# Optimization experiments

Measured on AMD Instinct MI355X. Metric: run time of the kernel, lower is better.

The kernel has to match this reference:

```python
import jax, jax.numpy as jnp
import numpy as np

EPS = 1e-6

def _ln2d(x, w, b):
    # LayerNorm2d: normalize over channel dim per pixel
    mu = x.mean(axis=1, keepdims=True)
    var = ((x - mu) ** 2).mean(axis=1, keepdims=True)
    return (x - mu) / jnp.sqrt(var + EPS) * w[None, :, None, None] + b[None, :, None, None]

def _conv1x1(x, w, b):
    return jnp.einsum('oc,bchw->bohw', w, x) + b[None, :, None, None]

def setup_inputs() -> dict:
    key = jax.random.key(0)
    ks = jax.random.split(key, 20)
    B, c, H, W = 4, 32, 256, 256
    dw = 2 * c
    k, wH, wW = 3, 32, 32
    s = 0.05
    d = {}
    d['inp'] = jax.random.normal(ks[0], (B, c, H, W), jnp.float32)
    d['conv2_weight'] = jax.random.normal(ks[1], (B, dw, k, k, wH, wW), jnp.float32) * 0.1
    d['conv1_w'] = jax.random.normal(ks[2], (dw, c), jnp.float32) * s
    d['conv1_b'] = jnp.zeros((dw,), jnp.float32)
    d['conv3_w'] = jax.random.normal(ks[3], (c, c), jnp.float32) * s
    d['conv3_b'] = jnp.zeros((c,), jnp.float32)
    d['sca_w'] = jax.random.normal(ks[4], (c, c), jnp.float32) * s
    d['sca_b'] = jnp.zeros((c,), jnp.float32)
    d['conv4_w'] = jax.random.normal(ks[5], (dw, c), jnp.float32) * s
    d['conv4_b'] = jnp.zeros((dw,), jnp.float32)
    d['conv5_w'] = jax.random.normal(ks[6], (c, c), jnp.float32) * s
    d['conv5_b'] = jnp.zeros((c,), jnp.float32)
    d['norm1_w'] = jnp.ones((c,), jnp.float32)
    d['norm1_b'] = jnp.zeros((c,), jnp.float32)
    d['norm2_w'] = jnp.ones((c,), jnp.float32)
    d['norm2_b'] = jnp.zeros((c,), jnp.float32)
    # original inits these to zero; use small random so the block is non-trivial
    d['beta'] = jax.random.normal(ks[7], (1, c, 1, 1), jnp.float32) * 0.1
    d['gamma'] = jax.random.normal(ks[8], (1, c, 1, 1), jnp.float32) * 0.1
    return d

def reference(inp, conv2_weight, conv1_w, conv1_b, conv3_w, conv3_b, sca_w, sca_b,
              conv4_w, conv4_b, conv5_w, conv5_b, norm1_w, norm1_b, norm2_w, norm2_b,
              beta, gamma):
    B, c, H, W = inp.shape
    x = _ln2d(inp, norm1_w, norm1_b)
    x = _conv1x1(x, conv1_w, conv1_b)                 # [B, 2c, H, W]
    Bw, C, kH, kW, wH, wW = conv2_weight.shape
    # bilinear upsample (half-pixel centers, == torch align_corners=False)
    w2 = conv2_weight.reshape(B * C, kH * kW, wH, wW)
    w2 = jax.image.resize(w2, (B * C, kH * kW, H, W), method='linear')
    w2 = w2.reshape(B, C, kH * kW, H, W)
    # ddf with all-ones channel filter + 'mul' == per-pixel spatial 3x3 conv per channel
    pad = kH // 2
    xp = jnp.pad(x, ((0, 0), (0, 0), (pad, pad), (pad, pad)))
    patches = jnp.stack([xp[:, :, i:i + H, j:j + W]
                         for i in range(kH) for j in range(kW)], axis=2)  # [B,2c,9,H,W]
    x = (patches * w2).sum(axis=2)                    # [B, 2c, H, W]
    x1, x2 = jnp.split(x, 2, axis=1)                  # SimpleGate
    x = x1 * x2                                       # [B, c, H, W]
    s = _conv1x1(x.mean(axis=(2, 3), keepdims=True), sca_w, sca_b)
    x = x * s
    x = _conv1x1(x, conv3_w, conv3_b)
    y = inp + x * beta
    x = _conv1x1(_ln2d(y, norm2_w, norm2_b), conv4_w, conv4_b)
    x1, x2 = jnp.split(x, 2, axis=1)
    x = _conv1x1(x1 * x2, conv5_w, conv5_b)
    return y + x * gamma
```

## Files before the change

### kernel.cpp

```cpp
#include <hip/hip_runtime.h>
#include <hip/hip_bf16.h>

typedef __hip_bfloat16 bf16;
typedef __attribute__((ext_vector_type(8))) unsigned short u16x8;
typedef __attribute__((ext_vector_type(8))) short s16x8;
typedef __attribute__((ext_vector_type(4))) float f32x4;
typedef __attribute__((ext_vector_type(4))) unsigned short us16x4;

#define B_   4
#define C_   32
#define DW_  64
#define H_   256
#define W_   256
#define P_   65536
#define SRC_ 32
#define TRS_ 272
#define TPL_ 70176

#define OW1    0
#define OB1    2048
#define OW3    2112
#define OB3    3136
#define OWS    3168
#define OBS    4192
#define OW4    4224
#define OB4    6272
#define OW5    6336
#define OB5    7360
#define ON1W   7392
#define ON1B   7424
#define ON2W   7456
#define ON2B   7488
#define OBETA  7520
#define OGAMMA 7552
#define OSUMS  7584
#define OSVEC  7712
#define OFLAG  7900
#define CWF_BOFF 32768ull
#define T1_BOFF  (CWF_BOFF + 9437184ull)
#define G_BOFF   (T1_BOFF + 35930112ull)

__device__ __forceinline__ bf16  f2b(float v){ return __float2bfloat16(v); }
__device__ __forceinline__ float bfu(unsigned short u){ return __uint_as_float(((unsigned int)u) << 16); }
__device__ __forceinline__ unsigned short fbits(float v){
    bf16 b = __float2bfloat16(v);
    return *reinterpret_cast<unsigned short*>(&b);
}

template<typename T> __device__ __forceinline__ float ldf(const T* p);
template<> __device__ __forceinline__ float ldf<float>(const float* p){ return *p; }
template<> __device__ __forceinline__ float ldf<bf16>(const bf16* p){ return __bfloat162float(*p); }

template<typename T> __device__ __forceinline__ void stf(T* p, float v);
template<> __device__ __forceinline__ void stf<float>(float* p, float v){ *p = v; }
template<> __device__ __forceinline__ void stf<bf16>(bf16* p, float v){ *p = __float2bfloat16(v); }

template<typename T> struct dtag;
template<> struct dtag<float>{ static constexpr int v = 0; };
template<> struct dtag<bf16>{ static constexpr int v = 1; };

__device__ __forceinline__ f32x4 MF(s16x8 a, s16x8 b, f32x4 c){
    return __builtin_amdgcn_mfma_f32_16x16x32_bf16(a, b, c, 0, 0, 0);
}
__device__ __forceinline__ s16x8 wfrag8(const float* p){
    float4 a = *(const float4*)p;
    float4 c = *(const float4*)(p + 4);
    s16x8 r;
    r[0] = (short)fbits(a.x); r[1] = (short)fbits(a.y);
    r[2] = (short)fbits(a.z); r[3] = (short)fbits(a.w);
    r[4] = (short)fbits(c.x); r[5] = (short)fbits(c.y);
    r[6] = (short)fbits(c.z); r[7] = (short)fbits(c.w);
    return r;
}

__global__ void k_detect(const unsigned short* __restrict__ raw, int* __restrict__ flag)
{
    int t = threadIdx.x;
    int bad = 0;
    for (int k = 0; k < 8; ++k) {
        unsigned short u = raw[2 * (t + 64 * k)];
        float v = __uint_as_float(((unsigned int)u) << 16);
        if (!(fabsf(v) < 1e6f)) bad = 1;
    }
    int anybad = __any(bad);
    if (t == 0) *flag = anybad ? 0 : 1;
}

template<typename T>
__global__ void k_prep(const T* __restrict__ w1, const T* __restrict__ b1,
                       const T* __restrict__ w3, const T* __restrict__ b3,
                       const T* __restrict__ wsc, const T* __restrict__ bsc_,
                       const T* __restrict__ w4, const T* __restrict__ b4,
                       const T* __restrict__ w5, const T* __restrict__ b5,
                       const T* __restrict__ n1w, const T* __restrict__ n1b,
                       const T* __restrict__ n2w, const T* __restrict__ n2b,
                       const T* __restrict__ bet, const T* __restrict__ gam,
                       float* __restrict__ wsf, const int* __restrict__ flag)
{
    if (*flag != dtag<T>::v) return;
    int t = threadIdx.x;
    for (int i = t; i < 2048; i += 256) wsf[OW1 + i] = ldf<T>(w1 + i);
    for (int i = t; i < 64;   i += 256) wsf[OB1 + i] = ldf<T>(b1 + i);
    for (int i = t; i < 1024; i += 256) wsf[OW3 + i] = ldf<T>(w3 + i);
    for (int i = t; i < 32;   i += 256) wsf[OB3 + i] = ldf<T>(b3 + i);
    for (int i = t; i < 1024; i += 256) wsf[OWS + i] = ldf<T>(wsc + i);
    for (int i = t; i < 32;   i += 256) wsf[OBS + i] = ldf<T>(bsc_ + i);
    for (int i = t; i < 2048; i += 256) wsf[OW4 + i] = ldf<T>(w4 + i);
    for (int i = t; i < 64;   i += 256) wsf[OB4 + i] = ldf<T>(b4 + i);
    for (int i = t; i < 1024; i += 256) wsf[OW5 + i] = ldf<T>(w5 + i);
    for (int i = t; i < 32;   i += 256) wsf[OB5 + i] = ldf<T>(b5 + i);
    for (int i = t; i < 32;   i += 256) wsf[ON1W + i] = ldf<T>(n1w + i);
    for (int i = t; i < 32;   i += 256) wsf[ON1B + i] = ldf<T>(n1b + i);
    for (int i = t; i < 32;   i += 256) wsf[ON2W + i] = ldf<T>(n2w + i);
    for (int i = t; i < 32;   i += 256) wsf[ON2B + i] = ldf<T>(n2b + i);
    for (int i = t; i < 32;   i += 256) wsf[OBETA + i] = ldf<T>(bet + i);
    for (int i = t; i < 32;   i += 256) wsf[OGAMMA + i] = ldf<T>(gam + i);
    for (int i = t; i < 128;  i += 256) wsf[OSUMS + i] = 0.f;
}

__global__ void k_cwf(const void* __restrict__ cw, float4* __restrict__ cwf4,
                      const int* __restrict__ flag)
{
    int i4 = blockIdx.x * 256 + threadIdx.x;
    if (*flag == 0) {
        cwf4[i4] = ((const float4*)cw)[i4];
    } else {
        const ushort4* p = (const ushort4*)cw;
        ushort4 v = p[i4];
        cwf4[i4] = make_float4(bfu(v.x), bfu(v.y), bfu(v.z), bfu(v.w));
    }
}

__global__ void k_zpad(unsigned short* __restrict__ t1u)
{
    unsigned short* pl = t1u + (size_t)blockIdx.x * TPL_;
    int t = threadIdx.x;
    for (int i = t; i < 258; i += 256) {
        pl[i] = 0;
        pl[257 * TRS_ + i] = 0;
    }
    pl[(t + 1) * TRS_] = 0;
    pl[(t + 1) * TRS_ + 257] = 0;
}

template<typename T>
__device__ __forceinline__ void ln1_body(const T* __restrict__ inp,
        const float* __restrict__ wsf, bf16* __restrict__ t1p, short* __restrict__ xsh)
{
    const int t = threadIdx.x;
    const int b = blockIdx.x >> 8;
    const int p0 = (blockIdx.x & 255) << 8;

    {
        const T* ip = inp + (size_t)(b * C_) * P_ + p0 + t;
        float v[C_];
        float m = 0.f;
        #pragma unroll
        for (int ch = 0; ch < C_; ++ch) { v[ch] = ldf<T>(ip + (size_t)ch * P_); m += v[ch]; }
        m *= (1.f / C_);
        float var = 0.f;
        #pragma unroll
        for (int ch = 0; ch < C_; ++ch) { float d = v[ch] - m; var += d * d; }
        var *= (1.f / C_);
        float inv = rsqrtf(var + 1e-6f);
        u16x8* xr = (u16x8*)(xsh + t * 32);
        #pragma unroll
        for (int qq = 0; qq < 4; ++qq) {
            u16x8 vv;
            #pragma unroll
            for (int j = 0; j < 8; ++j) {
                int ch = qq * 8 + j;
                vv[j] = fbits((v[ch] - m) * inv * wsf[ON1W + ch] + wsf[ON1B + ch]);
            }
            xr[qq] = vv;
        }
    }
    __syncthreads();

    const int lane = t & 63, wv = t >> 6;
    const int l15 = lane & 15, l4 = lane >> 4;
    const int wp0 = wv * 64;

    s16x8 w1f[4];
    f32x4 b1v[4];
    #pragma unroll
    for (int m = 0; m < 4; ++m) {
        w1f[m] = wfrag8(wsf + OW1 + (m * 16 + l15) * 32 + l4 * 8);
        b1v[m] = *(const f32x4*)(wsf + OB1 + m * 16 + l4 * 4);
    }

    const int h = p0 >> 8;
    bf16* op = t1p + (size_t)(b * DW_) * TPL_ + (size_t)(h + 1) * TRS_ + 1;
    #pragma unroll
    for (int tn = 0; tn < 4; ++tn) {
        int px = wp0 + tn * 16 + l15;
        s16x8 xb = *(const s16x8*)(xsh + px * 32 + l4 * 8);
        #pragma unroll
        for (int m = 0; m < 4; ++m) {
            f32x4 acc = MF(w1f[m], xb, b1v[m]);
            #pragma unroll
            for (int i = 0; i < 4; ++i) {
                int och = m * 16 + l4 * 4 + i;
                op[(size_t)och * TPL_ + px] = f2b(acc[i]);
            }
        }
    }
}

__global__ __launch_bounds__(256, 4) void k_ln1_conv1(const void* __restrict__ inp,
        const float* __restrict__ wsf, bf16* __restrict__ t1p,
        const int* __restrict__ flag)
{
    __shared__ short xsh[256 * 32];
    if (*flag == 0) ln1_body<float>((const float*)inp, wsf, t1p, xsh);
    else            ln1_body<bf16>((const bf16*)inp, wsf, t1p, xsh);
}

#define G_ 4
__global__ __launch_bounds__(256, 4) void k_ddf(const unsigned short* __restrict__ t1u,
        const float* __restrict__ cwf, bf16* __restrict__ g, float* __restrict__ sums)
{
    __shared__ float CWs[4320];

    int bid = blockIdx.x;
    int tile = bid & 31;
    int cg  = (bid >> 5) & 7;
    int b   = bid >> 8;
    int th = tile >> 2, tw = tile & 3;
    int cellh0 = th * 4;
    int cellw0 = tw * 8;
    int cp0 = cg * G_;

    {
        const float* cb = cwf + (size_t)b * (DW_ * 9 * 1024);
        for (int it = 0; it < 17; ++it) {
            int idx = it * 256 + threadIdx.x;
            if (idx < 4320) {
                int cc  = idx % 10;
                int t2  = idx / 10;
                int rr  = t2 % 6;
                int t3  = t2 / 6;
                int tap = t3 % 9;
                int chl = t3 / 9;
                int ch = (chl < G_) ? (cp0 + chl) : (C_ + cp0 + chl - G_);
                int cr = cellh0 - 1 + rr; cr = cr < 0 ? 0 : (cr > 31 ? 31 : cr);
                int cw = cellw0 - 1 + cc; cw = cw < 0 ? 0 : (cw > 31 ? 31 : cw);
                CWs[idx] = cb[ch * 9216 + tap * 1024 + cr * SRC_ + cw];
            }
        }
    }
    __syncthreads();

    int lane = threadIdx.x & 63, wid = threadIdx.x >> 6;
    int k = lane >> 3, r = lane & 7;
    int cellh = cellh0 + wid;
    int h = cellh * 8 + r;
    int w = (cellw0 + k) * 8;

    int rsel = r >> 2;
    float fh = rsel ? ((float)r * 0.125f - 0.4375f) : ((float)r * 0.125f + 0.5625f);
    float gh = 1.f - fh;
    int rr0k = (wid + rsel) * 10 + k;

    const unsigned short* tb = t1u + (size_t)(b * DW_) * TPL_ + (size_t)h * TRS_ + w;
    bf16* gp = g + (size_t)(b * C_) * P_ + h * 256 + w;

    for (int l = 0; l < G_; ++l) {
        int cp = cp0 + l;
        const unsigned short* pl1 = tb + (size_t)cp * TPL_;
        const unsigned short* pl2 = pl1 + (size_t)C_ * TPL_;
        const float* q1 = CWs + l * 540;
        const float* q2 = CWs + (G_ + l) * 540;

        float acc1[8], acc2[8];
        #pragma unroll
        for (int pass = 0; pass < 2; ++pass) {
            const unsigned short* pl = pass ? pl2 : pl1;
            const float* q = pass ? q2 : q1;
            float* acc = pass ? acc2 : acc1;

            u16x8 v8[3];
            unsigned int ve[3];
            #pragma unroll
            for (int i = 0; i < 3; ++i) {
                const unsigned short* rp = pl + i * TRS_;
                v8[i] = *(const u16x8*)rp;
                ve[i] = *(const unsigned int*)(rp + 8);
            }
            float S00[8], S01[8], S10[8], S11[8];
            #pragma unroll
            for (int c = 0; c < 8; ++c) { S00[c]=0.f; S01[c]=0.f; S10[c]=0.f; S11[c]=0.f; }
            #pragma unroll
            for (int i = 0; i < 3; ++i) {
                float p[10];
                #pragma unroll
                for (int j = 0; j < 8; ++j) p[j] = bfu((unsigned short)v8[i][j]);
                p[8] = bfu((unsigned short)(ve[i] & 0xFFFFu));
                p[9] = bfu((unsigned short)(ve[i] >> 16));
                #pragma unroll
                for (int j = 0; j < 3; ++j) {
                    const float* qb = q + (i * 3 + j) * 60 + rr0k;
                    float w00 = qb[0],  w01 = qb[1],  w02 = qb[2];
                    float w10 = qb[10], w11 = qb[11], w12 = qb[12];
                    #pragma unroll
                    for (int c = 0; c < 8; ++c) {
                        float pv = p[c + j];
                        S00[c] += pv * ((c < 4) ? w00 : w01);
                        S01[c] += pv * ((c < 4) ? w01 : w02);
                        S10[c] += pv * ((c < 4) ? w10 : w11);
                        S11[c] += pv * ((c < 4) ? w11 : w12);
                    }
                }
            }
            const float fwt[8] = {0.5625f, 0.6875f, 0.8125f, 0.9375f,
                                  0.0625f, 0.1875f, 0.3125f, 0.4375f};
            #pragma unroll
            for (int c = 0; c < 8; ++c) {
                float fw = fwt[c], gw = 1.f - fw;
                acc[c] = gh * (gw * S00[c] + fw * S01[c]) + fh * (gw * S10[c] + fw * S11[c]);
            }
        }

        u16x8 ov;
        float s = 0.f;
        #pragma unroll
        for (int c = 0; c < 8; ++c) {
            float gv = acc1[c] * acc2[c];
            s += gv;
            bf16 bv = f2b(gv);
            ov[c] = *reinterpret_cast<unsigned short*>(&bv);
        }
        *(u16x8*)(gp + (size_t)cp * P_) = ov;

        #pragma unroll
        for (int off = 32; off >= 1; off >>= 1) s += __shfl_xor(s, off, 64);
        if (lane == 0) atomicAdd(&sums[b * C_ + cp], s);
    }
}

__global__ void k_sca(float* __restrict__ wsf)
{
    int t = threadIdx.x;
    int b = t >> 5, o = t & 31;
    float acc = wsf[OBS + o];
    #pragma unroll
    for (int ch = 0; ch < C_; ++ch)
        acc += wsf[OWS + o * C_ + ch] * (wsf[OSUMS + b * C_ + ch] * (1.f / (float)P_));
    wsf[OSVEC + b * C_ + o] = acc;
}

#define XSTR_ 32
#define ISTR_ 33

template<typename T>
__device__ __forceinline__ void tail_body(const T* __restrict__ inp,
        const bf16* __restrict__ g, const float* __restrict__ wsf,
        T* __restrict__ out, short* __restrict__ xsh, float* __restrict__ ipsh)
{
    const int t = threadIdx.x;
    const int b = blockIdx.x >> 8;
    const int p0 = (blockIdx.x & 255) << 8;

    {
        float sv[32];
        #pragma unroll
        for (int q = 0; q < 8; ++q) {
            float4 v = *(const float4*)(wsf + OSVEC + b * 32 + q * 4);
            sv[4*q+0] = v.x; sv[4*q+1] = v.y; sv[4*q+2] = v.z; sv[4*q+3] = v.w;
        }
        const unsigned short* gp = (const unsigned short*)g + (size_t)(b * C_) * P_ + p0 + t;
        unsigned short row[32];
        #pragma unroll
        for (int ch = 0; ch < C_; ++ch)
            row[ch] = fbits(bfu(gp[(size_t)ch * P_]) * sv[ch]);
        u16x8* xr = (u16x8*)(xsh + t * XSTR_);
        #pragma unroll
        for (int qq = 0; qq < 4; ++qq) {
            u16x8 vv;
            #pragma unroll
            for (int j = 0; j < 8; ++j) vv[j] = row[qq * 8 + j];
            xr[qq] = vv;
        }
        const T* ip = inp + (size_t)(b * C_) * P_ + p0 + t;
        float* ir = ipsh + t * ISTR_;
        #pragma unroll
        for (int ch = 0; ch < C_; ++ch)
            ir[ch] = ldf<T>(ip + (size_t)ch * P_);
    }
    __syncthreads();

    const int lane = t & 63, wv = t >> 6;
    const int l15 = lane & 15, l4 = lane >> 4;
    const int wp0 = wv * 64;

    s16x8 w3f[2], w4f[4];
    #pragma unroll
    for (int m = 0; m < 2; ++m) w3f[m] = wfrag8(wsf + OW3 + (m * 16 + l15) * 32 + l4 * 8);
    #pragma unroll
    for (int m = 0; m < 4; ++m) w4f[m] = wfrag8(wsf + OW4 + (m * 16 + l15) * 32 + l4 * 8);

    f32x4 y[2][4];
    {
        f32x4 b3v[2], btv[2];
        #pragma unroll
        for (int m = 0; m < 2; ++m) {
            b3v[m] = *(const f32x4*)(wsf + OB3   + m * 16 + l4 * 4);
            btv[m] = *(const f32x4*)(wsf + OBETA + m * 16 + l4 * 4);
        }
        #pragma unroll
        for (int tn = 0; tn < 4; ++tn) {
            int px = wp0 + tn * 16 + l15;
            s16x8 xb = *(const s16x8*)(xsh + px * XSTR_ + l4 * 8);
            const float* irr = ipsh + px * ISTR_ + l4 * 4;
            #pragma unroll
            for (int m = 0; m < 2; ++m) {
                f32x4 acc = MF(w3f[m], xb, b3v[m]);
                f32x4 yy;
                #pragma unroll
                for (int i = 0; i < 4; ++i)
                    yy[i] = irr[m * 16 + i] + acc[i] * btv[m][i];
                y[m][tn] = yy;
            }
        }
    }

    {
        f32x4 nwv[2], nbv[2];
        #pragma unroll
        for (int m = 0; m < 2; ++m) {
            nwv[m] = *(const f32x4*)(wsf + ON2W + m * 16 + l4 * 4);
            nbv[m] = *(const f32x4*)(wsf + ON2B + m * 16 + l4 * 4);
        }
        #pragma unroll
        for (int tn = 0; tn < 4; ++tn) {
            float s = 0.f;
            #pragma unroll
            for (int m = 0; m < 2; ++m)
                #pragma unroll
                for (int i = 0; i < 4; ++i) s += y[m][tn][i];
            s += __shfl_xor(s, 16);
            s += __shfl_xor(s, 32);
            float mean = s * (1.f / 32.f);
            float q = 0.f;
            #pragma unroll
            for (int m = 0; m < 2; ++m)
                #pragma unroll
                for (int i = 0; i < 4; ++i) { float d = y[m][tn][i] - mean; q += d * d; }
            q += __shfl_xor(q, 16);
            q += __shfl_xor(q, 32);
            float inv = rsqrtf(q * (1.f / 32.f) + 1e-6f);
            int px = wp0 + tn * 16 + l15;
            #pragma unroll
            for (int m = 0; m < 2; ++m) {
                us16x4 pk;
                #pragma unroll
                for (int i = 0; i < 4; ++i)
                    pk[i] = fbits((y[m][tn][i] - mean) * inv * nwv[m][i] + nbv[m][i]);
                *(us16x4*)(xsh + px * XSTR_ + m * 16 + l4 * 4) = pk;
            }
        }
    }

    {
        f32x4 b4v[4];
        #pragma unroll
        for (int m = 0; m < 4; ++m)
            b4v[m] = *(const f32x4*)(wsf + OB4 + m * 16 + l4 * 4);
        s16x8 yb[4];
        #pragma unroll
        for (int tn = 0; tn < 4; ++tn)
            yb[tn] = *(const s16x8*)(xsh + (wp0 + tn * 16 + l15) * XSTR_ + l4 * 8);
        #pragma unroll
        for (int tn = 0; tn < 4; ++tn) {
            f32x4 a4[4];
            #pragma unroll
            for (int m = 0; m < 4; ++m) a4[m] = MF(w4f[m], yb[tn], b4v[m]);
            int px = wp0 + tn * 16 + l15;
            #pragma unroll
            for (int m = 0; m < 2; ++m) {
                us16x4 pk;
                #pragma unroll
                for (int i = 0; i < 4; ++i) pk[i] = fbits(a4[m][i] * a4[m + 2][i]);
                *(us16x4*)(xsh + px * XSTR_ + m * 16 + l4 * 4) = pk;
            }
        }
    }

    {
        s16x8 w5f[2];
        #pragma unroll
        for (int m = 0; m < 2; ++m) w5f[m] = wfrag8(wsf + OW5 + (m * 16 + l15) * 32 + l4 * 8);
        f32x4 b5v[2], gmv[2];
        #pragma unroll
        for (int m = 0; m < 2; ++m) {
            b5v[m] = *(const f32x4*)(wsf + OB5    + m * 16 + l4 * 4);
            gmv[m] = *(const f32x4*)(wsf + OGAMMA + m * 16 + l4 * 4);
        }
        s16x8 ub[4];
        #pragma unroll
        for (int tn = 0; tn < 4; ++tn)
            ub[tn] = *(const s16x8*)(xsh + (wp0 + tn * 16 + l15) * XSTR_ + l4 * 8);
        #pragma unroll
        for (int tn = 0; tn < 4; ++tn) {
            int px = p0 + wp0 + tn * 16 + l15;
            #pragma unroll
            for (int m = 0; m < 2; ++m) {
                f32x4 acc = MF(w5f[m], ub[tn], b5v[m]);
                #pragma unroll
                for (int i = 0; i < 4; ++i) {
                    int och = m * 16 + l4 * 4 + i;
                    stf<T>(out + (size_t)(b * C_ + och) * P_ + px,
                           y[m][tn][i] + acc[i] * gmv[m][i]);
                }
            }
        }
    }
}

__global__ __launch_bounds__(256, 3) void k_tail(const void* __restrict__ inp,
        const bf16* __restrict__ g, const float* __restrict__ wsf,
        void* __restrict__ out, const int* __restrict__ flag)
{
    __shared__ short xsh[256 * XSTR_];
    __shared__ float ipsh[256 * ISTR_];
    if (*flag == 0) tail_body<float>((const float*)inp, g, wsf, (float*)out, xsh, ipsh);
    else            tail_body<bf16>((const bf16*)inp, g, wsf, (bf16*)out, xsh, ipsh);
}

extern "C" void kernel_launch(void* const* d_in, const int* in_sizes, int n_in,
                              void* d_out, int out_size, void* d_ws, size_t ws_size,
                              hipStream_t stream)
{
    float* wsf = (float*)d_ws;
    char* wsb = (char*)d_ws;
    float* cwf = (float*)(wsb + CWF_BOFF);
    bf16* t1p = (bf16*)(wsb + T1_BOFF);
    bf16* g   = (bf16*)(wsb + G_BOFF);
    int* flag = (int*)(wsf + OFLAG);

    k_detect<<<1, 64, 0, stream>>>((const unsigned short*)d_in[0], flag);

    int nblk = (B_ * P_) / 256;

    k_prep<float><<<1, 256, 0, stream>>>(
        (const float*)d_in[2], (const float*)d_in[3], (const float*)d_in[4],
        (const float*)d_in[5], (const float*)d_in[6], (const float*)d_in[7],
        (const float*)d_in[8], (const float*)d_in[9], (const float*)d_in[10],
        (const float*)d_in[11], (const float*)d_in[12], (const float*)d_in[13],
        (const float*)d_in[14], (const float*)d_in[15], (const float*)d_in[16],
        (const float*)d_in[17], wsf, flag);
    k_prep<bf16><<<1, 256, 0, stream>>>(
        (const bf16*)d_in[2], (const bf16*)d_in[3], (const bf16*)d_in[4],
        (const bf16*)d_in[5], (const bf16*)d_in[6], (const bf16*)d_in[7],
        (const bf16*)d_in[8], (const bf16*)d_in[9], (const bf16*)d_in[10],
        (const bf16*)d_in[11], (const bf16*)d_in[12], (const bf16*)d_in[13],
        (const bf16*)d_in[14], (const bf16*)d_in[15], (const bf16*)d_in[16],
        (const bf16*)d_in[17], wsf, flag);

    k_cwf<<<2304, 256, 0, stream>>>(d_in[1], (float4*)cwf, flag);

    k_zpad<<<256, 256, 0, stream>>>((unsigned short*)t1p);

    k_ln1_conv1<<<nblk, 256, 0, stream>>>(d_in[0], wsf, t1p, flag);

    k_ddf<<<1024, 256, 0, stream>>>((const unsigned short*)t1p, cwf, g, wsf + OSUMS);

    k_sca<<<1, 128, 0, stream>>>(wsf);

    k_tail<<<nblk, 256, 0, stream>>>(d_in[0], g, wsf, d_out, flag);
}
```

Before: 238.1 us.

## Stage conv1 and tail outputs through LDS for coalesced stores, fold zpad and sca

conv1 results now go to shared memory and are written out as full padded rows with 16-byte vector stores, including the zero halo columns. The top and bottom pad rows are zeroed by the edge blocks, so the separate zero-pad kernel is removed. The SCA vector is computed per block inside the tail kernel, which removes the k_sca launch. The tail's final output is staged through LDS for vectorized, coalesced writes. This trades extra barriers and LDS traffic for fewer scattered 2-byte and 4-byte global stores and two fewer launches.

```diff
diff --git a/kernel.cpp b/kernel.cpp
--- a/kernel.cpp
+++ b/kernel.cpp
@@ -51,10 +51,6 @@
 template<> __device__ __forceinline__ float ldf<float>(const float* p){ return *p; }
 template<> __device__ __forceinline__ float ldf<bf16>(const bf16* p){ return __bfloat162float(*p); }
 
-template<typename T> __device__ __forceinline__ void stf(T* p, float v);
-template<> __device__ __forceinline__ void stf<float>(float* p, float v){ *p = v; }
-template<> __device__ __forceinline__ void stf<bf16>(bf16* p, float v){ *p = __float2bfloat16(v); }
-
 template<typename T> struct dtag;
 template<> struct dtag<float>{ static constexpr int v = 0; };
 template<> struct dtag<bf16>{ static constexpr int v = 1; };
@@ -131,25 +127,16 @@
     }
 }
 
-__global__ void k_zpad(unsigned short* __restrict__ t1u)
-{
-    unsigned short* pl = t1u + (size_t)blockIdx.x * TPL_;
-    int t = threadIdx.x;
-    for (int i = t; i < 258; i += 256) {
-        pl[i] = 0;
-        pl[257 * TRS_ + i] = 0;
-    }
-    pl[(t + 1) * TRS_] = 0;
-    pl[(t + 1) * TRS_ + 257] = 0;
-}
-
+#define OSTR1_ 280
 template<typename T>
 __device__ __forceinline__ void ln1_body(const T* __restrict__ inp,
-        const float* __restrict__ wsf, bf16* __restrict__ t1p, short* __restrict__ xsh)
+        const float* __restrict__ wsf, bf16* __restrict__ t1p,
+        short* __restrict__ xsh, short* __restrict__ osh)
 {
     const int t = threadIdx.x;
     const int b = blockIdx.x >> 8;
-    const int p0 = (blockIdx.x & 255) << 8;
+    const int h = blockIdx.x & 255;
+    const int p0 = h << 8;
 
     {
         const T* ip = inp + (size_t)(b * C_) * P_ + p0 + t;
@@ -174,6 +161,8 @@
             }
             xr[qq] = vv;
         }
+        int och = t >> 4, cc = t & 15;
+        osh[och * OSTR1_ + (cc == 0 ? 0 : 256 + cc)] = 0;
     }
     __syncthreads();
 
@@ -188,20 +177,44 @@
         w1f[m] = wfrag8(wsf + OW1 + (m * 16 + l15) * 32 + l4 * 8);
         b1v[m] = *(const f32x4*)(wsf + OB1 + m * 16 + l4 * 4);
     }
-
-    const int h = p0 >> 8;
-    bf16* op = t1p + (size_t)(b * DW_) * TPL_ + (size_t)(h + 1) * TRS_ + 1;
+    s16x8 xb[4];
     #pragma unroll
-    for (int tn = 0; tn < 4; ++tn) {
-        int px = wp0 + tn * 16 + l15;
-        s16x8 xb = *(const s16x8*)(xsh + px * 32 + l4 * 8);
-        #pragma unroll
-        for (int m = 0; m < 4; ++m) {
-            f32x4 acc = MF(w1f[m], xb, b1v[m]);
-            #pragma unroll
-            for (int i = 0; i < 4; ++i) {
-                int och = m * 16 + l4 * 4 + i;
-                op[(size_t)och * TPL_ + px] = f2b(acc[i]);
+    for (int tn = 0; tn < 4; ++tn)
+        xb[tn] = *(const s16x8*)(xsh + (wp0 + tn * 16 + l15) * 32 + l4 * 8);
+
+    const size_t prow = (size_t)(b * DW_) * TPL_ + (size_t)(h + 1) * TRS_;
+    #pragma unroll
+    for (int m = 0; m < 4; ++m) {
+        #pragma unroll
+        for (int tn = 0; tn < 4; ++tn) {
+            f32x4 acc = MF(w1f[m], xb[tn], b1v[m]);
+            int px = wp0 + tn * 16 + l15;
+            #pragma unroll
+            for (int i = 0; i < 4; ++i)
+                osh[(l4 * 4 + i) * OSTR1_ + 1 + px] = (short)fbits(acc[i]);
+        }
+        __syncthreads();
+        for (int it = 0; it < 3; ++it) {
+            int idx = it * 256 + t;
+            if (idx < 544) {
+                int och = idx / 34, ck = idx - och * 34;
+                u16x8 v = *(const u16x8*)(osh + och * OSTR1_ + ck * 8);
+                *(u16x8*)((unsigned short*)t1p + prow + (size_t)(m * 16 + och) * TPL_ + ck * 8) = v;
+            }
+        }
+        __syncthreads();
+    }
+
+    if (h == 0 || h == 255) {
+        size_t rbase = (size_t)(b * DW_) * TPL_ + (h == 0 ? 0 : (size_t)257 * TRS_);
+        u16x8 z;
+        #pragma unroll
+        for (int j = 0; j < 8; ++j) z[j] = 0;
+        for (int it = 0; it < 9; ++it) {
+            int idx = it * 256 + t;
+            if (idx < 2176) {
+                int och = idx / 34, ck = idx - och * 34;
+                *(u16x8*)((unsigned short*)t1p + rbase + (size_t)och * TPL_ + ck * 8) = z;
             }
         }
     }
@@ -212,8 +225,9 @@
         const int* __restrict__ flag)
 {
     __shared__ short xsh[256 * 32];
-    if (*flag == 0) ln1_body<float>((const float*)inp, wsf, t1p, xsh);
-    else            ln1_body<bf16>((const bf16*)inp, wsf, t1p, xsh);
+    __shared__ short osh[16 * OSTR1_];
+    if (*flag == 0) ln1_body<float>((const float*)inp, wsf, t1p, xsh, osh);
+    else            ln1_body<bf16>((const bf16*)inp, wsf, t1p, xsh, osh);
 }
 
 #define G_ 4
@@ -338,41 +352,35 @@
     }
 }
 
-__global__ void k_sca(float* __restrict__ wsf)
-{
-    int t = threadIdx.x;
-    int b = t >> 5, o = t & 31;
-    float acc = wsf[OBS + o];
-    #pragma unroll
-    for (int ch = 0; ch < C_; ++ch)
-        acc += wsf[OWS + o * C_ + ch] * (wsf[OSUMS + b * C_ + ch] * (1.f / (float)P_));
-    wsf[OSVEC + b * C_ + o] = acc;
-}
-
 #define XSTR_ 32
 #define ISTR_ 33
+#define OSTRT_ 260
 
 template<typename T>
 __device__ __forceinline__ void tail_body(const T* __restrict__ inp,
         const bf16* __restrict__ g, const float* __restrict__ wsf,
-        T* __restrict__ out, short* __restrict__ xsh, float* __restrict__ ipsh)
+        T* __restrict__ out, short* __restrict__ xsh, float* __restrict__ ipsh,
+        float* __restrict__ svsh)
 {
     const int t = threadIdx.x;
     const int b = blockIdx.x >> 8;
     const int p0 = (blockIdx.x & 255) << 8;
 
-    {
-        float sv[32];
-        #pragma unroll
-        for (int q = 0; q < 8; ++q) {
-            float4 v = *(const float4*)(wsf + OSVEC + b * 32 + q * 4);
-            sv[4*q+0] = v.x; sv[4*q+1] = v.y; sv[4*q+2] = v.z; sv[4*q+3] = v.w;
-        }
+    if (t < 32) {
+        float acc = wsf[OBS + t];
+        #pragma unroll
+        for (int ch = 0; ch < C_; ++ch)
+            acc += wsf[OWS + t * C_ + ch] * (wsf[OSUMS + b * C_ + ch] * (1.f / (float)P_));
+        svsh[t] = acc;
+    }
+    __syncthreads();
+
+    {
         const unsigned short* gp = (const unsigned short*)g + (size_t)(b * C_) * P_ + p0 + t;
         unsigned short row[32];
         #pragma unroll
         for (int ch = 0; ch < C_; ++ch)
-            row[ch] = fbits(bfu(gp[(size_t)ch * P_]) * sv[ch]);
+            row[ch] = fbits(bfu(gp[(size_t)ch * P_]) * svsh[ch]);
         u16x8* xr = (u16x8*)(xsh + t * XSTR_);
         #pragma unroll
         for (int qq = 0; qq < 4; ++qq) {
@@ -423,6 +431,7 @@
             }
         }
     }
+    __syncthreads();
 
     {
         f32x4 nwv[2], nbv[2];
@@ -500,18 +509,44 @@
         #pragma unroll
         for (int tn = 0; tn < 4; ++tn)
             ub[tn] = *(const s16x8*)(xsh + (wp0 + tn * 16 + l15) * XSTR_ + l4 * 8);
+        float* oshf = ipsh;
         #pragma unroll
         for (int tn = 0; tn < 4; ++tn) {
-            int px = p0 + wp0 + tn * 16 + l15;
+            int px = wp0 + tn * 16 + l15;
             #pragma unroll
             for (int m = 0; m < 2; ++m) {
                 f32x4 acc = MF(w5f[m], ub[tn], b5v[m]);
                 #pragma unroll
-                for (int i = 0; i < 4; ++i) {
-                    int och = m * 16 + l4 * 4 + i;
-                    stf<T>(out + (size_t)(b * C_ + och) * P_ + px,
-                           y[m][tn][i] + acc[i] * gmv[m][i]);
-                }
+                for (int i = 0; i < 4; ++i)
+                    oshf[(m * 16 + l4 * 4 + i) * OSTRT_ + px] = y[m][tn][i] + acc[i] * gmv[m][i];
+            }
+        }
+    }
+    __syncthreads();
+
+    {
+        const float* oshf = ipsh;
+        if (dtag<T>::v == 0) {
+            float* of = (float*)out;
+            #pragma unroll
+            for (int it = 0; it < 8; ++it) {
+                int idx = it * 256 + t;
+                int och = idx >> 6, ck = idx & 63;
+                f32x4 v = *(const f32x4*)(oshf + och * OSTRT_ + ck * 4);
+                *(f32x4*)(of + (size_t)(b * C_ + och) * P_ + p0 + ck * 4) = v;
+            }
+        } else {
+            unsigned short* ob = (unsigned short*)out;
+            #pragma unroll
+            for (int it = 0; it < 4; ++it) {
+                int idx = it * 256 + t;
+                int och = idx >> 5, ck = idx & 31;
+                f32x4 a = *(const f32x4*)(oshf + och * OSTRT_ + ck * 8);
+                f32x4 c = *(const f32x4*)(oshf + och * OSTRT_ + ck * 8 + 4);
+                u16x8 pk;
+                pk[0] = fbits(a[0]); pk[1] = fbits(a[1]); pk[2] = fbits(a[2]); pk[3] = fbits(a[3]);
+                pk[4] = fbits(c[0]); pk[5] = fbits(c[1]); pk[6] = fbits(c[2]); pk[7] = fbits(c[3]);
+                *(u16x8*)(ob + (size_t)(b * C_ + och) * P_ + p0 + ck * 8) = pk;
             }
         }
     }
@@ -523,8 +558,9 @@
 {
     __shared__ short xsh[256 * XSTR_];
     __shared__ float ipsh[256 * ISTR_];
-    if (*flag == 0) tail_body<float>((const float*)inp, g, wsf, (float*)out, xsh, ipsh);
-    else            tail_body<bf16>((const bf16*)inp, g, wsf, (bf16*)out, xsh, ipsh);
+    __shared__ float svsh[32];
+    if (*flag == 0) tail_body<float>((const float*)inp, g, wsf, (float*)out, xsh, ipsh, svsh);
+    else            tail_body<bf16>((const bf16*)inp, g, wsf, (bf16*)out, xsh, ipsh, svsh);
 }
 
 extern "C" void kernel_launch(void* const* d_in, const int* in_sizes, int n_in,
@@ -559,13 +595,9 @@
 
     k_cwf<<<2304, 256, 0, stream>>>(d_in[1], (float4*)cwf, flag);
 
-    k_zpad<<<256, 256, 0, stream>>>((unsigned short*)t1p);
-
     k_ln1_conv1<<<nblk, 256, 0, stream>>>(d_in[0], wsf, t1p, flag);
 
     k_ddf<<<1024, 256, 0, stream>>>((const unsigned short*)t1p, cwf, g, wsf + OSUMS);
 
-    k_sca<<<1, 128, 0, stream>>>(wsf);
-
     k_tail<<<nblk, 256, 0, stream>>>(d_in[0], g, wsf, d_out, flag);
 }
```

Result: faster. 232.0 us (-2.6%).
